# Performance work log

Hardware: AMD Instinct MI355X
Metric: run time of the kernel (lower is better)

Reference implementation:

```python
import jax, jax.numpy as jnp
import numpy as np
from jax import lax

N, C, S_CH = 16, 256, 512  # batch, content channels (c_in=c_out), style channels
DN = ('NCHW', 'OIHW', 'NCHW')


def setup_inputs() -> dict:
    key = jax.random.key(0)
    ks = jax.random.split(key, 8)
    p = lambda k, s: jax.random.normal(k, s, jnp.float32) * 0.05
    return {
        'style_encoding': jax.random.normal(ks[0], (N, S_CH, 4, 4), jnp.float32),
        'content_in': jax.random.normal(ks[1], (N, C, 64, 64), jnp.float32),
        # depthwise_kernel_conv: Conv2d(512, n_groups=1, kernel=2)
        'dw_w': p(ks[2], (1, S_CH, 2, 2)), 'dw_b': p(ks[3], (1,)),
        # pw_cn_kn: Conv2d(512, pointwise_groups=1, 1)
        'pw_kn_w': p(ks[4], (1, S_CH, 1, 1)), 'pw_kn_b': p(ks[5], (1,)),
        # pw_cn_bias: Conv2d(512, c_out=256, 1)
        'pw_bias_w': p(ks[6], (C, S_CH, 1, 1)), 'pw_bias_b': p(ks[7], (C,)),
    }


def reference(style_encoding, content_in, dw_w, dw_b, pw_kn_w, pw_kn_b, pw_bias_w, pw_bias_b):
    n = style_encoding.shape[0]
    # depthwise kernel prediction: (N,1,3,3) -> expand -> (N, c_out, c_in, 3, 3)
    dk = lax.conv_general_dilated(style_encoding, dw_w, (1, 1), 'VALID',
                                  dimension_numbers=DN) + dw_b[None, :, None, None]
    depthwise = jnp.broadcast_to(dk[:, None], (n, C, C, 3, 3))
    # AvgPool2d(4) on 4x4 spatial == global mean -> (N,512,1,1)
    s_d = jnp.mean(style_encoding, axis=(2, 3))  # (N,512)
    # 1x1 convs on 1x1 spatial are plain matmuls
    pw1 = s_d @ pw_kn_w[:, :, 0, 0].T + pw_kn_b              # (N,1)
    pointwise_kn = jnp.broadcast_to(pw1[:, None, :, None, None], (n, C, C, 1, 1))
    pointwise_bias = s_d @ pw_bias_w[:, :, 0, 0].T + pw_bias_b  # (N,256)
    # ReflectionPad2d((1,1,1,1))
    x = jnp.pad(content_in, ((0, 0), (0, 0), (1, 1), (1, 1)), mode='reflect')

    def sample_conv(xi, wi, pwi, bi):
        # xi: (C,H+2,W+2), wi: (C,C,3,3) dynamic per-sample weight (groups=1)
        d = lax.conv_general_dilated(xi[None], wi, (1, 1), 'VALID',
                                     dimension_numbers=DN)[0]  # (C,H,W)
        # pointwise 1x1 conv with per-sample weight + bias
        return jnp.einsum('oi,ihw->ohw', pwi[:, :, 0, 0], d) + bi[:, None, None]

    return jax.vmap(sample_conv)(x, depthwise, pointwise_kn, pointwise_bias)
```

## Files before the change

### kernel.cpp

```cpp
#include <hip/hip_runtime.h>


#define OFF_SCALE 0
#define OFF_K     16
#define OFF_SD    160
#define OFF_XP    8352

__global__ __launch_bounds__(256, 2) void ada_front(
    const float* __restrict__ style,
    const float* __restrict__ content,
    const float* __restrict__ dw_w,
    const float* __restrict__ dw_b,
    const float* __restrict__ pw_kn_w,
    const float* __restrict__ pw_kn_b,
    float* __restrict__ ws)
{
    const int t = threadIdx.x;
    __shared__ float red[4][10];

    if (blockIdx.x >= 16) {
        const int b  = blockIdx.x - 16;
        const int n  = b >> 5;
        const int g  = (b >> 2) & 7;
        const int pt = b & 3;
        const int p4 = pt * 256 + t;

        const float4* src = (const float4*)content
                          + ((size_t)(n * 256 + g * 32)) * 1024 + p4;
        float4 a = make_float4(0.f, 0.f, 0.f, 0.f);
#pragma unroll 8
        for (int c = 0; c < 32; ++c) {
            float4 v = src[(size_t)c * 1024];
            a.x += v.x; a.y += v.y; a.z += v.z; a.w += v.w;
        }
        ((float4*)(ws + OFF_XP))[((size_t)(n * 8 + g)) * 1024 + p4] = a;
        return;
    }

    const int n = blockIdx.x;

    float acc[10];
#pragma unroll
    for (int j = 0; j < 10; ++j) acc[j] = 0.f;

#pragma unroll
    for (int cc = 0; cc < 2; ++cc) {
        const int c = t + cc * 256;
        const float4* sp = (const float4*)(style + ((size_t)n * 512 + c) * 16);
        float v[16];
#pragma unroll
        for (int q = 0; q < 4; ++q) {
            float4 f = sp[q];
            v[q*4+0] = f.x; v[q*4+1] = f.y; v[q*4+2] = f.z; v[q*4+3] = f.w;
        }
        float sum = 0.f;
#pragma unroll
        for (int q = 0; q < 16; ++q) sum += v[q];
        const float sdc = sum * 0.0625f;
        ws[OFF_SD + n * 512 + c] = sdc;

        const float* w = dw_w + c * 4;
        const float w00 = w[0], w01 = w[1], w10 = w[2], w11 = w[3];
#pragma unroll
        for (int ki = 0; ki < 3; ++ki)
#pragma unroll
            for (int kj = 0; kj < 3; ++kj)
                acc[ki*3+kj] += v[ki*4 + kj]       * w00
                              + v[ki*4 + kj + 1]   * w01
                              + v[(ki+1)*4 + kj]   * w10
                              + v[(ki+1)*4 + kj+1] * w11;
        acc[9] += sdc * pw_kn_w[c];
    }

#pragma unroll
    for (int off = 32; off >= 1; off >>= 1)
#pragma unroll
        for (int j = 0; j < 10; ++j)
            acc[j] += __shfl_down(acc[j], off, 64);

    if ((t & 63) == 0) {
#pragma unroll
        for (int j = 0; j < 10; ++j) red[t >> 6][j] = acc[j];
    }
    __syncthreads();

    if (t < 10) {
        const float s = red[0][t] + red[1][t] + red[2][t] + red[3][t];
        if (t < 9) ws[OFF_K + n * 9 + t] = s + dw_b[0];
        else       ws[OFF_SCALE + n]     = 256.f * (s + pw_kn_b[0]);
    }
}

__global__ __launch_bounds__(256, 2) void ada_back(
    const float* __restrict__ ws,
    const float* __restrict__ pw_bias_w,
    const float* __restrict__ pw_bias_b,
    float4* __restrict__ out)
{
    const int bid = blockIdx.x;
    const int n   = bid >> 6;
    const int s   = bid & 63;
    const int t   = threadIdx.x;

    __shared__ float Xs[4096];
    __shared__ float E[4096];
    __shared__ float sdl[512];
    __shared__ float bias_s[4];

    if (t < 128)
        ((float4*)sdl)[t] = ((const float4*)(ws + OFF_SD + (size_t)n * 512))[t];

    const float4* Xp = (const float4*)(ws + OFF_XP) + (size_t)n * 8 * 1024;
#pragma unroll
    for (int i = 0; i < 4; ++i) {
        const int p4 = i * 256 + t;
        float4 a = Xp[p4];
#pragma unroll
        for (int g = 1; g < 8; ++g) {
            float4 v = Xp[g * 1024 + p4];
            a.x += v.x; a.y += v.y; a.z += v.z; a.w += v.w;
        }
        ((float4*)Xs)[p4] = a;
    }

    float k[9];
#pragma unroll
    for (int j = 0; j < 9; ++j) k[j] = ws[OFF_K + n * 9 + j];
    const float scale = ws[OFF_SCALE + n];
    __syncthreads();

    {
        const int wv = t >> 6, l = t & 63;
        const int o  = s * 4 + wv;
        const float4* wr = (const float4*)(pw_bias_w + (size_t)o * 512);
        const float4 a0 = wr[l * 2];
        const float4 a1 = wr[l * 2 + 1];
        const float4 s0 = *(const float4*)&sdl[l * 8];
        const float4 s1 = *(const float4*)&sdl[l * 8 + 4];
        float d = a0.x*s0.x + a0.y*s0.y + a0.z*s0.z + a0.w*s0.w
                + a1.x*s1.x + a1.y*s1.y + a1.z*s1.z + a1.w*s1.w;
#pragma unroll
        for (int off = 32; off >= 1; off >>= 1)
            d += __shfl_down(d, off, 64);
        if (l == 0) bias_s[wv] = d + pw_bias_b[o];
    }

#pragma unroll
    for (int r = 0; r < 16; ++r) {
        const int p = r * 256 + t, h = p >> 6, w = p & 63;
        float d = 0.f;
#pragma unroll
        for (int ki = 0; ki < 3; ++ki) {
            int hh = h + ki - 1;
            hh = hh < 0 ? 1 : (hh > 63 ? 62 : hh);
#pragma unroll
            for (int kj = 0; kj < 3; ++kj) {
                int wwi = w + kj - 1;
                wwi = wwi < 0 ? 1 : (wwi > 63 ? 62 : wwi);
                d += k[ki*3+kj] * Xs[hh * 64 + wwi];
            }
        }
        E[p] = scale * d;
    }
    __syncthreads();

    const float4* E4 = (const float4*)E;
    float4* o = out + ((size_t)(n * 256 + s * 4)) * 1024;
#pragma unroll
    for (int pl = 0; pl < 4; ++pl) {
        const float b = bias_s[pl];
#pragma unroll
        for (int i = 0; i < 4; ++i) {
            float4 v = E4[i * 256 + t];
            o[(size_t)pl * 1024 + i * 256 + t] =
                make_float4(v.x + b, v.y + b, v.z + b, v.w + b);
        }
    }
}

extern "C" void kernel_launch(void* const* d_in, const int* in_sizes, int n_in,
                              void* d_out, int out_size, void* d_ws, size_t ws_size,
                              hipStream_t stream)
{
    const float* style     = (const float*)d_in[0];
    const float* content   = (const float*)d_in[1];
    const float* dw_w      = (const float*)d_in[2];
    const float* dw_b      = (const float*)d_in[3];
    const float* pw_kn_w   = (const float*)d_in[4];
    const float* pw_kn_b   = (const float*)d_in[5];
    const float* pw_bias_w = (const float*)d_in[6];
    const float* pw_bias_b = (const float*)d_in[7];
    float*  ws  = (float*)d_ws;
    float4* out = (float4*)d_out;

    ada_front<<<16 + 512, 256, 0, stream>>>(style, content, dw_w, dw_b,
                                            pw_kn_w, pw_kn_b, ws);
    ada_back <<<1024,     256, 0, stream>>>(ws, pw_bias_w, pw_bias_b, out);
}
```

Baseline: 34.59 us.

## Compute stencil in registers with float4 rows and write outputs directly

Result: faster. 31.03 us (-10.3%).

```diff
diff --git a/kernel.cpp b/kernel.cpp
--- a/kernel.cpp
+++ b/kernel.cpp
@@ -103,12 +103,22 @@
     const int t   = threadIdx.x;
 
     __shared__ float Xs[4096];
-    __shared__ float E[4096];
-    __shared__ float sdl[512];
     __shared__ float bias_s[4];
 
-    if (t < 128)
-        ((float4*)sdl)[t] = ((const float4*)(ws + OFF_SD + (size_t)n * 512))[t];
+    {
+        const int wv = t >> 6, l = t & 63;
+        const int o  = s * 4 + wv;
+        const float4* wr = (const float4*)(pw_bias_w + (size_t)o * 512);
+        const float4* sv = (const float4*)(ws + OFF_SD + (size_t)n * 512);
+        const float4 a0 = wr[l * 2],     a1 = wr[l * 2 + 1];
+        const float4 s0 = sv[l * 2],     s1 = sv[l * 2 + 1];
+        float d = a0.x*s0.x + a0.y*s0.y + a0.z*s0.z + a0.w*s0.w
+                + a1.x*s1.x + a1.y*s1.y + a1.z*s1.z + a1.w*s1.w;
+#pragma unroll
+        for (int off = 32; off >= 1; off >>= 1)
+            d += __shfl_down(d, off, 64);
+        if (l == 0) bias_s[wv] = d + pw_bias_b[o];
+    }
 
     const float4* Xp = (const float4*)(ws + OFF_XP) + (size_t)n * 8 * 1024;
 #pragma unroll
@@ -129,52 +139,36 @@
     const float scale = ws[OFF_SCALE + n];
     __syncthreads();
 
-    {
-        const int wv = t >> 6, l = t & 63;
-        const int o  = s * 4 + wv;
-        const float4* wr = (const float4*)(pw_bias_w + (size_t)o * 512);
-        const float4 a0 = wr[l * 2];
-        const float4 a1 = wr[l * 2 + 1];
-        const float4 s0 = *(const float4*)&sdl[l * 8];
-        const float4 s1 = *(const float4*)&sdl[l * 8 + 4];
-        float d = a0.x*s0.x + a0.y*s0.y + a0.z*s0.z + a0.w*s0.w
-                + a1.x*s1.x + a1.y*s1.y + a1.z*s1.z + a1.w*s1.w;
-#pragma unroll
-        for (int off = 32; off >= 1; off >>= 1)
-            d += __shfl_down(d, off, 64);
-        if (l == 0) bias_s[wv] = d + pw_bias_b[o];
-    }
+    const float b0 = bias_s[0], b1 = bias_s[1], b2 = bias_s[2], b3 = bias_s[3];
+    float4* obase = out + ((size_t)(n * 256 + s * 4)) * 1024;
 
 #pragma unroll
-    for (int r = 0; r < 16; ++r) {
-        const int p = r * 256 + t, h = p >> 6, w = p & 63;
-        float d = 0.f;
+    for (int q = 0; q < 4; ++q) {
+        const int h  = q * 16 + (t >> 4);
+        const int w0 = (t & 15) * 4;
+        const int hm = (h == 0)  ? 1  : h - 1;
+        const int hp = (h == 63) ? 62 : h + 1;
+        float e0 = 0.f, e1 = 0.f, e2 = 0.f, e3 = 0.f;
+        const int rows[3] = { hm, h, hp };
 #pragma unroll
-        for (int ki = 0; ki < 3; ++ki) {
-            int hh = h + ki - 1;
-            hh = hh < 0 ? 1 : (hh > 63 ? 62 : hh);
-#pragma unroll
-            for (int kj = 0; kj < 3; ++kj) {
-                int wwi = w + kj - 1;
-                wwi = wwi < 0 ? 1 : (wwi > 63 ? 62 : wwi);
-                d += k[ki*3+kj] * Xs[hh * 64 + wwi];
-            }
+        for (int i = 0; i < 3; ++i) {
+            const float* R = &Xs[rows[i] * 64];
+            const float4 m    = *(const float4*)&R[w0];
+            const float  left  = (w0 == 0)  ? R[1]  : R[w0 - 1];
+            const float  right = (w0 == 60) ? R[62] : R[w0 + 4];
+            const float k0 = k[i*3], k1 = k[i*3+1], k2 = k[i*3+2];
+            e0 += k0*left + k1*m.x + k2*m.y;
+            e1 += k0*m.x  + k1*m.y + k2*m.z;
+            e2 += k0*m.y  + k1*m.z + k2*m.w;
+            e3 += k0*m.z  + k1*m.w + k2*right;
         }
-        E[p] = scale * d;
-    }
-    __syncthreads();
+        e0 *= scale; e1 *= scale; e2 *= scale; e3 *= scale;
 
-    const float4* E4 = (const float4*)E;
-    float4* o = out + ((size_t)(n * 256 + s * 4)) * 1024;
-#pragma unroll
-    for (int pl = 0; pl < 4; ++pl) {
-        const float b = bias_s[pl];
-#pragma unroll
-        for (int i = 0; i < 4; ++i) {
-            float4 v = E4[i * 256 + t];
-            o[(size_t)pl * 1024 + i * 256 + t] =
-                make_float4(v.x + b, v.y + b, v.z + b, v.w + b);
-        }
+        float4* o = obase + q * 256 + t;
+        o[0]    = make_float4(e0 + b0, e1 + b0, e2 + b0, e3 + b0);
+        o[1024] = make_float4(e0 + b1, e1 + b1, e2 + b1, e3 + b1);
+        o[2048] = make_float4(e0 + b2, e1 + b2, e2 + b2, e3 + b2);
+        o[3072] = make_float4(e0 + b3, e1 + b3, e2 + b3, e3 + b3);
     }
 }
 
```
